# Kernel optimization log

Hardware: AMD Instinct MI355X
Metric: run time of the kernel (lower is better)

## Reference

```python
import jax, jax.numpy as jnp
import numpy as np

_SCAN_CHUNK = 32


def _causal_decay_scan(x, decay, init):
    """Inclusive scan out[t] = decay*out[t-1] + x[t], chunked closed form.
    x: [B,H,T,D], decay: [1,H,1], init: [B,H,D]. Returns [B,H,T,D]."""
    B, H, T, D = x.shape
    C = min(_SCAN_CHUNK, T)
    assert T % C == 0
    nC = T // C
    log_decay = jnp.log(jnp.clip(decay.astype(jnp.float32), 1e-8, None))  # [1,H,1]
    c_idx = jnp.arange(C, dtype=jnp.float32)
    log_p = log_decay[..., None] * c_idx.reshape(1, 1, C, 1)              # [1,H,C,1]
    p = jnp.exp(log_p)
    inv_p = jnp.exp(-log_p)
    init_p = jnp.exp(log_decay[..., None] * (c_idx + 1.0).reshape(1, 1, C, 1))
    # [nC, B, H, C, D] so lax.scan chains chunk states causally
    xc = x.reshape(B, H, nC, C, D).transpose(2, 0, 1, 3, 4).astype(jnp.float32)

    def step(state, chunk):  # state [B,H,D], chunk [B,H,C,D]
        cs = jnp.cumsum(chunk * inv_p, axis=2)
        out = cs * p + state[:, :, None, :] * init_p
        return out[:, :, -1, :], out

    _, outs = jax.lax.scan(step, init.astype(jnp.float32), xc)
    return outs.transpose(1, 2, 0, 3, 4).reshape(B, H, T, D).astype(x.dtype)


def _phi(x):
    return jax.nn.elu(x) + 1.0


def setup_inputs() -> dict:
    key = jax.random.key(0)
    ks = jax.random.split(key, 5)
    B, T, hidden, H = 4, 4096, 1024, 16
    s = 1.0 / np.sqrt(hidden)
    x = jax.random.normal(ks[0], (B, T, hidden), dtype=jnp.float32)
    Wqkv = jax.random.normal(ks[1], (3 * hidden, hidden), dtype=jnp.float32) * s
    Wout = jax.random.normal(ks[2], (hidden, hidden), dtype=jnp.float32) * s
    Wgate = jax.random.normal(ks[3], (hidden, hidden), dtype=jnp.float32) * s
    bgate = jnp.zeros((hidden,), dtype=jnp.float32)
    logit = float(np.log(0.95 / 0.05))  # sigmoid(logit) == 0.95
    decay_param = jnp.full((H,), logit, dtype=jnp.float32)
    return {"x": x, "Wqkv": Wqkv, "Wout": Wout, "Wgate": Wgate,
            "bgate": bgate, "decay_param": decay_param}


def reference(x, Wqkv, Wout, Wgate, bgate, decay_param):
    B, T, hidden = x.shape
    H = decay_param.shape[0]
    D = hidden // H
    qkv = x @ Wqkv.T                       # [B,T,3*hidden]
    q, k, v = jnp.split(qkv, 3, axis=-1)
    # [B,T,hidden] -> [B,H,T,D]
    q = q.reshape(B, T, H, D).transpose(0, 2, 1, 3)
    k = k.reshape(B, T, H, D).transpose(0, 2, 1, 3)
    v = v.reshape(B, T, H, D).transpose(0, 2, 1, 3)
    q = _phi(q)
    k = _phi(k)
    decay = jax.nn.sigmoid(decay_param).reshape(1, H, 1)
    kv_init = jnp.zeros((B, H, D), dtype=x.dtype)
    ksum_init = jnp.zeros((B, H, D), dtype=x.dtype)
    running_kv = _causal_decay_scan(k * v, decay, kv_init)
    running_ksum = _causal_decay_scan(k, decay, ksum_init)
    den = jnp.clip(jnp.sum(q * running_ksum, axis=-1, keepdims=True), 1e-6, None)
    out = q * running_kv / den             # [B,H,T,D]
    v_direct = v.transpose(0, 2, 1, 3).reshape(B, T, hidden)
    out = out.transpose(0, 2, 1, 3).reshape(B, T, hidden)
    g = jax.nn.sigmoid(out @ Wgate.T + bgate)
    out = g * out + (1.0 - g) * v_direct
    return out @ Wout.T
```

## Files before the change

### kernel.cpp

```cpp
#include <hip/hip_runtime.h>

typedef unsigned short u16;
typedef __bf16 bf16x8 __attribute__((ext_vector_type(8)));
typedef float f32x4 __attribute__((ext_vector_type(4)));

#define BB 4
#define TT 4096
#define HID 1024
#define NH 16
#define HD 64
#define BT (BB*TT)
#define NCH 128
#define LOG_NCH 7
#define CLEN (TT/NCH)

__device__ __forceinline__ float bf2f(u16 u) {
    return __uint_as_float(((unsigned)u) << 16);
}
__device__ __forceinline__ u16 f2bf(float f) {
    unsigned u = __float_as_uint(f);
    unsigned r = 0x7FFFu + ((u >> 16) & 1u);
    return (u16)((u + r) >> 16);
}
__device__ __forceinline__ float phi(float x) {
    return x > 0.f ? x + 1.f : __expf(x);
}
__device__ __forceinline__ float sigmoidf(float x) {
    return 1.f / (1.f + __expf(-x));
}
__device__ __forceinline__ float4 u4_to_f4(ushort4 u) {
    return make_float4(bf2f(u.x), bf2f(u.y), bf2f(u.z), bf2f(u.w));
}

#define CN1 (BT*HID/4)
#define CN2 (3*HID*HID/4)
#define CN3 (HID*HID/4)
#define CN4 (HID*HID/4)
__global__ void convert_all(const float4* __restrict__ x,    const float4* __restrict__ wqkv,
                            const float4* __restrict__ wgate, const float4* __restrict__ wout,
                            ushort4* __restrict__ xb,    ushort4* __restrict__ wqkvb,
                            ushort4* __restrict__ wgateb, ushort4* __restrict__ woutb) {
    int i = blockIdx.x * 256 + threadIdx.x;
    const float4* src; ushort4* dst; int j;
    if (i < CN1)                 { src = x;     dst = xb;     j = i; }
    else if (i < CN1+CN2)        { src = wqkv;  dst = wqkvb;  j = i - CN1; }
    else if (i < CN1+CN2+CN3)    { src = wgate; dst = wgateb; j = i - CN1 - CN2; }
    else                         { src = wout;  dst = woutb;  j = i - CN1 - CN2 - CN3; }
    float4 f = src[j];
    ushort4 u;
    u.x = f2bf(f.x); u.y = f2bf(f.y); u.z = f2bf(f.z); u.w = f2bf(f.w);
    dst[j] = u;
}

template<int EPI>
__global__ __launch_bounds__(256)
void gemm_bt(const u16* __restrict__ A, const u16* __restrict__ Bm,
             int M, int N, int K, void* __restrict__ Cout,
             const float* __restrict__ bg,
             const u16* __restrict__ attn,
             const u16* __restrict__ qkv)
{
    __shared__ u16 As[128 * 64];
    __shared__ u16 Bs[128 * 64];
    const int tid  = threadIdx.x;
    const int wave = tid >> 6;
    const int lane = tid & 63;
    const int m0 = blockIdx.y * 128;
    const int n0 = blockIdx.x * 128;
    const int mw = (wave & 1) * 64;
    const int nw = (wave >> 1) * 64;
    const int r16 = lane & 15;

    f32x4 acc[4][4];
    #pragma unroll
    for (int i = 0; i < 4; ++i)
        #pragma unroll
        for (int j = 0; j < 4; ++j)
            acc[i][j] = (f32x4){0.f, 0.f, 0.f, 0.f};

    for (int k0 = 0; k0 < K; k0 += 64) {
        #pragma unroll
        for (int i = 0; i < 4; ++i) {
            int s   = i * 4 + wave;
            int idx = s * 64 + lane;
            int pr  = idx >> 3;
            int pc  = idx & 7;
            int lc  = pc ^ (pr & 7);
            const u16* gA = A  + (size_t)(m0 + pr) * K + k0 + lc * 8;
            const u16* gB = Bm + (size_t)(n0 + pr) * K + k0 + lc * 8;
            __builtin_amdgcn_global_load_lds(
                (const __attribute__((address_space(1))) void*)gA,
                (__attribute__((address_space(3))) void*)&As[s * 512], 16, 0, 0);
            __builtin_amdgcn_global_load_lds(
                (const __attribute__((address_space(1))) void*)gB,
                (__attribute__((address_space(3))) void*)&Bs[s * 512], 16, 0, 0);
        }
        __syncthreads();
        #pragma unroll
        for (int s2 = 0; s2 < 2; ++s2) {
            const int lcq = s2 * 4 + (lane >> 4);
            const int pcq = lcq ^ (r16 & 7);
            bf16x8 af[4], bq[4];
            #pragma unroll
            for (int i = 0; i < 4; ++i)
                af[i] = *(const bf16x8*)&As[(mw + i * 16 + r16) * 64 + pcq * 8];
            #pragma unroll
            for (int j = 0; j < 4; ++j)
                bq[j] = *(const bf16x8*)&Bs[(nw + j * 16 + r16) * 64 + pcq * 8];
            #pragma unroll
            for (int i = 0; i < 4; ++i)
                #pragma unroll
                for (int j = 0; j < 4; ++j)
                    acc[i][j] = __builtin_amdgcn_mfma_f32_16x16x32_bf16(af[i], bq[j], acc[i][j], 0, 0, 0);
        }
        __syncthreads();
    }

    #pragma unroll
    for (int i = 0; i < 4; ++i) {
        int rowb = m0 + mw + i * 16 + (lane >> 4) * 4;
        #pragma unroll
        for (int j = 0; j < 4; ++j) {
            int col = n0 + nw + j * 16 + r16;
            #pragma unroll
            for (int r = 0; r < 4; ++r) {
                float v = acc[i][j][r];
                size_t row = (size_t)(rowb + r);
                if (EPI == 0) {
                    ((u16*)Cout)[row * N + col] = f2bf(v);
                } else if (EPI == 1) {
                    float g  = sigmoidf(v + bg[col]);
                    float at = bf2f(attn[row * HID + col]);
                    float vd = bf2f(qkv[row * (3 * HID) + 2 * HID + col]);
                    ((u16*)Cout)[row * HID + col] = f2bf(g * at + (1.f - g) * vd);
                } else {
                    ((float*)Cout)[row * N + col] = v;
                }
            }
        }
    }
}

template<int EPI>
__global__ __launch_bounds__(256)
void gemm_bt_sm(const u16* __restrict__ A, const u16* __restrict__ Bm,
                int M, int N, int K, void* __restrict__ Cout,
                const float* __restrict__ bg,
                const u16* __restrict__ attn,
                const u16* __restrict__ qkv)
{
    __shared__ u16 As[64 * 64];
    __shared__ u16 Bs[128 * 64];
    const int tid  = threadIdx.x;
    const int wave = tid >> 6;
    const int lane = tid & 63;
    const int m0 = blockIdx.y * 64;
    const int n0 = blockIdx.x * 128;
    const int mw = (wave & 1) * 32;
    const int nw = (wave >> 1) * 64;
    const int r16 = lane & 15;

    f32x4 acc[2][4];
    #pragma unroll
    for (int i = 0; i < 2; ++i)
        #pragma unroll
        for (int j = 0; j < 4; ++j)
            acc[i][j] = (f32x4){0.f, 0.f, 0.f, 0.f};

    for (int k0 = 0; k0 < K; k0 += 64) {
        #pragma unroll
        for (int i = 0; i < 4; ++i) {
            int s   = i * 4 + wave;
            int idx = s * 64 + lane;
            int pr  = idx >> 3;
            int pc  = idx & 7;
            int lc  = pc ^ (pr & 7);
            const u16* gB = Bm + (size_t)(n0 + pr) * K + k0 + lc * 8;
            __builtin_amdgcn_global_load_lds(
                (const __attribute__((address_space(1))) void*)gB,
                (__attribute__((address_space(3))) void*)&Bs[s * 512], 16, 0, 0);
            if (i < 2) {
                const u16* gA = A + (size_t)(m0 + pr) * K + k0 + lc * 8;
                __builtin_amdgcn_global_load_lds(
                    (const __attribute__((address_space(1))) void*)gA,
                    (__attribute__((address_space(3))) void*)&As[s * 512], 16, 0, 0);
            }
        }
        __syncthreads();
        #pragma unroll
        for (int s2 = 0; s2 < 2; ++s2) {
            const int lcq = s2 * 4 + (lane >> 4);
            const int pcq = lcq ^ (r16 & 7);
            bf16x8 af[2], bq[4];
            #pragma unroll
            for (int i = 0; i < 2; ++i)
                af[i] = *(const bf16x8*)&As[(mw + i * 16 + r16) * 64 + pcq * 8];
            #pragma unroll
            for (int j = 0; j < 4; ++j)
                bq[j] = *(const bf16x8*)&Bs[(nw + j * 16 + r16) * 64 + pcq * 8];
            #pragma unroll
            for (int i = 0; i < 2; ++i)
                #pragma unroll
                for (int j = 0; j < 4; ++j)
                    acc[i][j] = __builtin_amdgcn_mfma_f32_16x16x32_bf16(af[i], bq[j], acc[i][j], 0, 0, 0);
        }
        __syncthreads();
    }

    #pragma unroll
    for (int i = 0; i < 2; ++i) {
        int rowb = m0 + mw + i * 16 + (lane >> 4) * 4;
        #pragma unroll
        for (int j = 0; j < 4; ++j) {
            int col = n0 + nw + j * 16 + r16;
            #pragma unroll
            for (int r = 0; r < 4; ++r) {
                float v = acc[i][j][r];
                size_t row = (size_t)(rowb + r);
                if (EPI == 1) {
                    float g  = sigmoidf(v + bg[col]);
                    float at = bf2f(attn[row * HID + col]);
                    float vd = bf2f(qkv[row * (3 * HID) + 2 * HID + col]);
                    ((u16*)Cout)[row * HID + col] = f2bf(g * at + (1.f - g) * vd);
                } else {
                    ((float*)Cout)[row * N + col] = v;
                }
            }
        }
    }
}

__global__ void scan_finals(const u16* __restrict__ qkv, const float* __restrict__ decay_param,
                            float* __restrict__ ckv, float* __restrict__ cks) {
    int g  = blockIdx.x * 16 + (threadIdx.x >> 4);
    int sl = threadIdx.x & 15;
    int c = g & (NCH - 1);
    int h = (g >> LOG_NCH) & (NH - 1);
    int b = g >> (LOG_NCH + 4);
    float decay = sigmoidf(decay_param[h]);
    const u16* kp = qkv + (size_t)(b * TT + c * CLEN) * (3 * HID) + HID + h * HD + sl * 4;
    float4 skv = make_float4(0.f, 0.f, 0.f, 0.f);
    float4 sks = make_float4(0.f, 0.f, 0.f, 0.f);
    for (int t = 0; t < CLEN; ++t) {
        float4 k = u4_to_f4(*(const ushort4*)kp);
        float4 v = u4_to_f4(*(const ushort4*)(kp + HID));
        k.x = phi(k.x); k.y = phi(k.y); k.z = phi(k.z); k.w = phi(k.w);
        skv.x = decay * skv.x + k.x * v.x;  skv.y = decay * skv.y + k.y * v.y;
        skv.z = decay * skv.z + k.z * v.z;  skv.w = decay * skv.w + k.w * v.w;
        sks.x = decay * sks.x + k.x;        sks.y = decay * sks.y + k.y;
        sks.z = decay * sks.z + k.z;        sks.w = decay * sks.w + k.w;
        kp += 3 * HID;
    }
    *(float4*)(ckv + (size_t)g * 64 + sl * 4) = skv;
    *(float4*)(cks + (size_t)g * 64 + sl * 4) = sks;
}

__global__ void scan_prefix(float* __restrict__ ckv, float* __restrict__ cks,
                            const float* __restrict__ decay_param) {
    int bh = blockIdx.x;
    int h  = bh & (NH - 1);
    int lane = threadIdx.x;
    float decay = sigmoidf(decay_param[h]);
    float dC = powf(decay, (float)CLEN);
    float* pkv = ckv + (size_t)bh * NCH * 64 + lane;
    float* pks = cks + (size_t)bh * NCH * 64 + lane;
    float fkv = 0.f, fks = 0.f;
    for (int c = 0; c < NCH; ++c) {
        float lkv = pkv[c * 64], lks = pks[c * 64];
        pkv[c * 64] = fkv; pks[c * 64] = fks;
        fkv = fkv * dC + lkv;
        fks = fks * dC + lks;
    }
}

__global__ void scan_apply(const u16* __restrict__ qkv, const float* __restrict__ decay_param,
                           const float* __restrict__ ckv, const float* __restrict__ cks,
                           u16* __restrict__ attn) {
    int g  = blockIdx.x * 16 + (threadIdx.x >> 4);
    int sl = threadIdx.x & 15;
    int c = g & (NCH - 1);
    int h = (g >> LOG_NCH) & (NH - 1);
    int b = g >> (LOG_NCH + 4);
    float decay = sigmoidf(decay_param[h]);
    float4 skv = *(const float4*)(ckv + (size_t)g * 64 + sl * 4);
    float4 sks = *(const float4*)(cks + (size_t)g * 64 + sl * 4);
    const u16* qp = qkv + (size_t)(b * TT + c * CLEN) * (3 * HID) + h * HD + sl * 4;
    u16* op = attn + (size_t)(b * TT + c * CLEN) * HID + h * HD + sl * 4;
    for (int t = 0; t < CLEN; ++t) {
        float4 q = u4_to_f4(*(const ushort4*)qp);
        float4 k = u4_to_f4(*(const ushort4*)(qp + HID));
        float4 v = u4_to_f4(*(const ushort4*)(qp + 2 * HID));
        q.x = phi(q.x); q.y = phi(q.y); q.z = phi(q.z); q.w = phi(q.w);
        k.x = phi(k.x); k.y = phi(k.y); k.z = phi(k.z); k.w = phi(k.w);
        skv.x = decay * skv.x + k.x * v.x;  skv.y = decay * skv.y + k.y * v.y;
        skv.z = decay * skv.z + k.z * v.z;  skv.w = decay * skv.w + k.w * v.w;
        sks.x = decay * sks.x + k.x;        sks.y = decay * sks.y + k.y;
        sks.z = decay * sks.z + k.z;        sks.w = decay * sks.w + k.w;
        float s = q.x * sks.x + q.y * sks.y + q.z * sks.z + q.w * sks.w;
        s += __shfl_xor(s, 8);
        s += __shfl_xor(s, 4);
        s += __shfl_xor(s, 2);
        s += __shfl_xor(s, 1);
        float inv = 1.f / fmaxf(s, 1e-6f);
        ushort4 o;
        o.x = f2bf(q.x * skv.x * inv); o.y = f2bf(q.y * skv.y * inv);
        o.z = f2bf(q.z * skv.z * inv); o.w = f2bf(q.w * skv.w * inv);
        *(ushort4*)op = o;
        qp += 3 * HID;
        op += HID;
    }
}

extern "C" void kernel_launch(void* const* d_in, const int* in_sizes, int n_in,
                              void* d_out, int out_size, void* d_ws, size_t ws_size,
                              hipStream_t stream) {
    const float* x     = (const float*)d_in[0];
    const float* Wqkv  = (const float*)d_in[1];
    const float* Wout  = (const float*)d_in[2];
    const float* Wgate = (const float*)d_in[3];
    const float* bgate = (const float*)d_in[4];
    const float* decay = (const float*)d_in[5];

    u16* xb     = (u16*)d_ws;
    u16* wqkvb  = xb    + (size_t)BT * HID;
    u16* wgateb = wqkvb + (size_t)3 * HID * HID;
    u16* woutb  = wgateb + (size_t)HID * HID;
    u16* qkvb   = woutb + (size_t)HID * HID;
    u16* out2b  = qkvb  + (size_t)BT * 3 * HID;
    float* ckv  = (float*)(out2b + (size_t)BT * HID);
    float* cks  = ckv + (size_t)BB * NH * NCH * HD;
    u16* attnb  = xb;

    convert_all<<<(CN1 + CN2 + CN3 + CN4) / 256, 256, 0, stream>>>(
        (const float4*)x, (const float4*)Wqkv, (const float4*)Wgate, (const float4*)Wout,
        (ushort4*)xb, (ushort4*)wqkvb, (ushort4*)wgateb, (ushort4*)woutb);

    gemm_bt<0><<<dim3(3 * HID / 128, BT / 128), 256, 0, stream>>>(
        xb, wqkvb, BT, 3 * HID, HID, qkvb, nullptr, nullptr, nullptr);

    scan_finals<<<BB * NH * NCH / 16, 256, 0, stream>>>(qkvb, decay, ckv, cks);
    scan_prefix<<<BB * NH, 64, 0, stream>>>(ckv, cks, decay);
    scan_apply<<<BB * NH * NCH / 16, 256, 0, stream>>>(qkvb, decay, ckv, cks, attnb);

    gemm_bt_sm<1><<<dim3(HID / 128, BT / 64), 256, 0, stream>>>(
        attnb, wgateb, BT, HID, HID, out2b, bgate, attnb, qkvb);

    gemm_bt_sm<2><<<dim3(HID / 128, BT / 64), 256, 0, stream>>>(
        out2b, woutb, BT, HID, HID, d_out, nullptr, nullptr, nullptr);
}
```

Before: 398.5 us.

## Stage GEMM epilogues through LDS for vectorized stores and remap blocks per XCD

The three GEMM kernels now stage accumulators through shared memory in 32-row slabs, so each thread writes 8 contiguous outputs per store instead of scattered 2-byte or 4-byte writes. The gated epilogue also reads attn and v with 16-byte vector loads. Block indices are remapped so each of the 8 XCDs gets a contiguous band of M rows, which should improve L2 reuse of A tiles. The cost is extra LDS traffic and barriers in the epilogue.

```diff
diff --git a/kernel.cpp b/kernel.cpp
--- a/kernel.cpp
+++ b/kernel.cpp
@@ -3,6 +3,7 @@
 typedef unsigned short u16;
 typedef __bf16 bf16x8 __attribute__((ext_vector_type(8)));
 typedef float f32x4 __attribute__((ext_vector_type(4)));
+typedef unsigned short us8 __attribute__((ext_vector_type(8)));
 
 #define BB 4
 #define TT 4096
@@ -52,24 +53,29 @@
     dst[j] = u;
 }
 
-template<int EPI>
 __global__ __launch_bounds__(256)
 void gemm_bt(const u16* __restrict__ A, const u16* __restrict__ Bm,
-             int M, int N, int K, void* __restrict__ Cout,
-             const float* __restrict__ bg,
-             const u16* __restrict__ attn,
-             const u16* __restrict__ qkv)
+             int M, int N, int K, u16* __restrict__ Cout)
 {
     __shared__ u16 As[128 * 64];
     __shared__ u16 Bs[128 * 64];
     const int tid  = threadIdx.x;
     const int wave = tid >> 6;
     const int lane = tid & 63;
-    const int m0 = blockIdx.y * 128;
-    const int n0 = blockIdx.x * 128;
+
+    const int lin   = blockIdx.y * gridDim.x + blockIdx.x;
+    const int xcd   = lin & 7;
+    const int seq   = lin >> 3;
+    const int bands = gridDim.y >> 3;
+    const int my_by = xcd * bands + (seq % bands);
+    const int my_bx = seq / bands;
+    const int m0 = my_by * 128;
+    const int n0 = my_bx * 128;
+
     const int mw = (wave & 1) * 64;
     const int nw = (wave >> 1) * 64;
     const int r16 = lane & 15;
+    const int q4  = (lane >> 4) * 4;
 
     f32x4 acc[4][4];
     #pragma unroll
@@ -116,28 +122,36 @@
         __syncthreads();
     }
 
+    float* Cs = (float*)As;
     #pragma unroll
-    for (int i = 0; i < 4; ++i) {
-        int rowb = m0 + mw + i * 16 + (lane >> 4) * 4;
-        #pragma unroll
-        for (int j = 0; j < 4; ++j) {
-            int col = n0 + nw + j * 16 + r16;
-            #pragma unroll
-            for (int r = 0; r < 4; ++r) {
-                float v = acc[i][j][r];
-                size_t row = (size_t)(rowb + r);
-                if (EPI == 0) {
-                    ((u16*)Cout)[row * N + col] = f2bf(v);
-                } else if (EPI == 1) {
-                    float g  = sigmoidf(v + bg[col]);
-                    float at = bf2f(attn[row * HID + col]);
-                    float vd = bf2f(qkv[row * (3 * HID) + 2 * HID + col]);
-                    ((u16*)Cout)[row * HID + col] = f2bf(g * at + (1.f - g) * vd);
-                } else {
-                    ((float*)Cout)[row * N + col] = v;
+    for (int slab = 0; slab < 4; ++slab) {
+        if ((mw == 64) == (slab >= 2)) {
+            int i0 = (slab & 1) * 2;
+            #pragma unroll
+            for (int ii = 0; ii < 2; ++ii) {
+                #pragma unroll
+                for (int j = 0; j < 4; ++j) {
+                    int col = nw + j * 16 + r16;
+                    #pragma unroll
+                    for (int r = 0; r < 4; ++r)
+                        Cs[(ii * 16 + q4 + r) * 128 + col] = acc[i0 + ii][j][r];
                 }
             }
         }
+        __syncthreads();
+        #pragma unroll
+        for (int s = 0; s < 2; ++s) {
+            int g   = s * 256 + tid;
+            int row = g >> 4;
+            int cg  = g & 15;
+            const float* cp = &Cs[row * 128 + cg * 8];
+            us8 o;
+            #pragma unroll
+            for (int e = 0; e < 8; ++e) o[e] = f2bf(cp[e]);
+            size_t grow = (size_t)(m0 + slab * 32 + row);
+            *(us8*)&Cout[grow * N + n0 + cg * 8] = o;
+        }
+        __syncthreads();
     }
 }
 
@@ -154,11 +168,20 @@
     const int tid  = threadIdx.x;
     const int wave = tid >> 6;
     const int lane = tid & 63;
-    const int m0 = blockIdx.y * 64;
-    const int n0 = blockIdx.x * 128;
+
+    const int lin   = blockIdx.y * gridDim.x + blockIdx.x;
+    const int xcd   = lin & 7;
+    const int seq   = lin >> 3;
+    const int bands = gridDim.y >> 3;
+    const int my_by = xcd * bands + (seq % bands);
+    const int my_bx = seq / bands;
+    const int m0 = my_by * 64;
+    const int n0 = my_bx * 128;
+
     const int mw = (wave & 1) * 32;
     const int nw = (wave >> 1) * 64;
     const int r16 = lane & 15;
+    const int q4  = (lane >> 4) * 4;
 
     f32x4 acc[2][4];
     #pragma unroll
@@ -207,26 +230,49 @@
         __syncthreads();
     }
 
+    float* Cs = (float*)Bs;
     #pragma unroll
-    for (int i = 0; i < 2; ++i) {
-        int rowb = m0 + mw + i * 16 + (lane >> 4) * 4;
-        #pragma unroll
-        for (int j = 0; j < 4; ++j) {
-            int col = n0 + nw + j * 16 + r16;
-            #pragma unroll
-            for (int r = 0; r < 4; ++r) {
-                float v = acc[i][j][r];
-                size_t row = (size_t)(rowb + r);
-                if (EPI == 1) {
-                    float g  = sigmoidf(v + bg[col]);
-                    float at = bf2f(attn[row * HID + col]);
-                    float vd = bf2f(qkv[row * (3 * HID) + 2 * HID + col]);
-                    ((u16*)Cout)[row * HID + col] = f2bf(g * at + (1.f - g) * vd);
-                } else {
-                    ((float*)Cout)[row * N + col] = v;
+    for (int slab = 0; slab < 2; ++slab) {
+        if ((wave & 1) == slab) {
+            #pragma unroll
+            for (int i = 0; i < 2; ++i) {
+                #pragma unroll
+                for (int j = 0; j < 4; ++j) {
+                    int col = nw + j * 16 + r16;
+                    #pragma unroll
+                    for (int r = 0; r < 4; ++r)
+                        Cs[(i * 16 + q4 + r) * 128 + col] = acc[i][j][r];
                 }
             }
         }
+        __syncthreads();
+        #pragma unroll
+        for (int s = 0; s < 2; ++s) {
+            int g   = s * 256 + tid;
+            int row = g >> 4;
+            int cg  = g & 15;
+            const float* cp = &Cs[row * 128 + cg * 8];
+            size_t grow = (size_t)(m0 + slab * 32 + row);
+            int gcol = n0 + cg * 8;
+            if (EPI == 1) {
+                us8 a8 = *(const us8*)&attn[grow * HID + gcol];
+                us8 v8 = *(const us8*)&qkv[grow * (3 * HID) + 2 * HID + gcol];
+                us8 o;
+                #pragma unroll
+                for (int e = 0; e < 8; ++e) {
+                    float gv = sigmoidf(cp[e] + bg[gcol + e]);
+                    o[e] = f2bf(gv * bf2f(a8[e]) + (1.f - gv) * bf2f(v8[e]));
+                }
+                *(us8*)&((u16*)Cout)[grow * HID + gcol] = o;
+            } else {
+                float4 c0 = *(const float4*)cp;
+                float4 c1 = *(const float4*)(cp + 4);
+                float* op = &((float*)Cout)[grow * N + gcol];
+                *(float4*)op = c0;
+                *(float4*)(op + 4) = c1;
+            }
+        }
+        __syncthreads();
     }
 }
 
@@ -335,8 +381,8 @@
         (const float4*)x, (const float4*)Wqkv, (const float4*)Wgate, (const float4*)Wout,
         (ushort4*)xb, (ushort4*)wqkvb, (ushort4*)wgateb, (ushort4*)woutb);
 
-    gemm_bt<0><<<dim3(3 * HID / 128, BT / 128), 256, 0, stream>>>(
-        xb, wqkvb, BT, 3 * HID, HID, qkvb, nullptr, nullptr, nullptr);
+    gemm_bt<<<dim3(3 * HID / 128, BT / 128), 256, 0, stream>>>(
+        xb, wqkvb, BT, 3 * HID, HID, qkvb);
 
     scan_finals<<<BB * NH * NCH / 16, 256, 0, stream>>>(qkvb, decay, ckv, cks);
     scan_prefix<<<BB * NH, 64, 0, stream>>>(ckv, cks, decay);
```

Result: slower. 423.5 us (+6.3%).
